# Kernel tuning notes

Hardware: AMD Instinct MI355X
Metric: run time of the kernel (lower is better)

The kernel has to match this reference:

```python
import jax, jax.numpy as jnp
import numpy as np

GRID = 16
N = GRID * GRID          # num_nodes = 256
D = 64                   # embed_dim
SPARSITY = 0.8
BATCH = 2048


def setup_inputs() -> dict:
    key = jax.random.key(0)
    ks = jax.random.split(key, 11)
    s1 = 1.0 / np.sqrt(D)          # fan_in of per-node Linears
    s2 = 1.0 / np.sqrt(N * D)      # fan_in of global_pool first Linear
    x = jax.random.normal(ks[0], (BATCH, N * D), dtype=jnp.float32)
    adj_param = jax.random.normal(ks[1], (N, N), dtype=jnp.float32) * 0.1
    W1 = jax.random.uniform(ks[2], (N, D, D), minval=-s1, maxval=s1, dtype=jnp.float32)
    b1 = jax.random.uniform(ks[3], (N, D), minval=-s1, maxval=s1, dtype=jnp.float32)
    W2 = jax.random.uniform(ks[4], (N, D, D), minval=-s1, maxval=s1, dtype=jnp.float32)
    b2 = jax.random.uniform(ks[5], (N, D), minval=-s1, maxval=s1, dtype=jnp.float32)
    gpW1 = jax.random.uniform(ks[6], (N * D, D), minval=-s2, maxval=s2, dtype=jnp.float32)
    gpb1 = jax.random.uniform(ks[7], (D,), minval=-s2, maxval=s2, dtype=jnp.float32)
    gpW2 = jax.random.uniform(ks[8], (D, D // 2), minval=-s1, maxval=s1, dtype=jnp.float32)
    gpb2 = jax.random.uniform(ks[9], (D // 2,), minval=-s1, maxval=s1, dtype=jnp.float32)
    return {"x": x, "adj_param": adj_param, "W1": W1, "b1": b1, "W2": W2, "b2": b2,
            "gpW1": gpW1, "gpb1": gpb1, "gpW2": gpW2, "gpb2": gpb2}


def _adjacency(adj_param):
    adj = jax.nn.sigmoid(adj_param)
    # threshold = sorted(flat adj)[int(sparsity * N*N)], then hard-threshold, then zero diagonal
    thr = jnp.sort(adj.reshape(-1))[int(SPARSITY * N * N)]
    adj = adj * (adj > thr)
    return adj * (1.0 - jnp.eye(N, dtype=adj.dtype))


def reference(x, adj_param, W1, b1, W2, b2, gpW1, gpb1, gpW2, gpb2):
    B = x.shape[0]
    adj = _adjacency(adj_param)
    xn = x.reshape(B, N, D)                                    # [B, N, D]
    # per-node distinct MLP == grouped GEMM with weights [N, D, D]
    h = jax.nn.relu(jnp.einsum('bnd,nde->bne', xn, W1) + b1)   # [B, N, D]
    node = jnp.einsum('bnd,nde->bne', h, W2) + b2              # [B, N, D]
    # adjacency-weighted neighbor sum: mixed[b,i] = sum_j adj[i,j] * node[b,j]
    mixed = jnp.einsum('ij,bjd->bid', adj, node)               # [B, N, D]
    final = 0.5 * mixed + 0.5 * node                           # residual mix
    g = jax.nn.relu(final.reshape(B, N * D) @ gpW1 + gpb1)     # [B, D]
    out = g @ gpW2 + gpb2                                      # [B, D//2]
    return out, adj
```

## Files before the change

kernel.cpp:

```cpp
#include <hip/hip_runtime.h>
#include <math.h>

typedef unsigned int uint;
typedef unsigned short ushort;
typedef short short8 __attribute__((ext_vector_type(8)));
typedef float f32x4 __attribute__((ext_vector_type(4)));

#define B_ 2048
#define N_ 256
#define D_ 64
#define ND_ 16384
#define NN_ 65536
#define KIDX_ 52428u
#define NGROUPS 16

#define WS_W1T    ((size_t)0)
#define WS_W2T    ((size_t)2*1024*1024)
#define WS_EFF    ((size_t)4*1024*1024)
#define WS_ADJT   ((size_t)6*1024*1024)
#define WS_GPARTS ((size_t)8*1024*1024)
#define WS_SCAL   ((size_t)16*1024*1024)

__device__ __forceinline__ ushort f2bf(float f) {
    uint u = __float_as_uint(f);
    u += 0x7fffu + ((u >> 16) & 1u);
    return (ushort)(u >> 16);
}
__device__ __forceinline__ float bf2f(ushort u) { return __uint_as_float(((uint)u) << 16); }

__device__ __forceinline__ float sigmoid_exact(float a) {
    float t = (float)exp(-(double)a);
    return 1.0f / (1.0f + t);
}

__device__ __forceinline__ int wfrag_off(int e, int k) {
    return ((((e >> 4) * 2 + (k >> 5)) * 4 + ((k >> 3) & 3)) * 16 + (e & 15)) * 8 + (k & 7);
}

__global__ __launch_bounds__(256) void k_convert(const float* __restrict__ W1,
                                                 const float* __restrict__ W2,
                                                 ushort* __restrict__ W1f,
                                                 ushort* __restrict__ W2f) {
    int bid = blockIdx.x, tid = threadIdx.x;
    __shared__ ushort P[4096] __attribute__((aligned(16)));
    const float* src = (bid < 256) ? W1 + (size_t)bid * 4096 : W2 + (size_t)(bid - 256) * 4096;
#pragma unroll
    for (int i = 0; i < 16; i++) {
        int idx = i * 256 + tid;
        int k = idx >> 6, e = idx & 63;
        P[wfrag_off(e, k)] = f2bf(src[idx]);
    }
    __syncthreads();
    ushort* dst = (bid < 256) ? W1f + (size_t)bid * 4096 : W2f + (size_t)(bid - 256) * 4096;
#pragma unroll
    for (int i = 0; i < 2; i++)
        ((uint4*)dst)[i * 256 + tid] = ((const uint4*)P)[i * 256 + tid];
}

__global__ __launch_bounds__(1024, 4) void k_radix_select(const float* __restrict__ adj_param,
                                                          uint* __restrict__ scal) {
    __shared__ uint histL[256 * 64];
    __shared__ uint wsum[4];
    __shared__ uint bc[2];
    int tid = threadIdx.x;
    int lane = tid & 63;
    uint prefix = 0;
    uint rank = KIDX_;
    const uint4* pv = (const uint4*)adj_param;
#pragma unroll 1
    for (int pass = 0; pass < 4; pass++) {
        int shift = 24 - 8 * pass;
        for (int i = tid; i < 256 * 64; i += 1024) histL[i] = 0u;
        __syncthreads();
#pragma unroll 1
        for (int i = 0; i < 16; i++) {
            uint4 b4 = pv[i * 1024 + tid];
#pragma unroll
            for (int c = 0; c < 4; c++) {
                uint bits = (c == 0) ? b4.x : (c == 1) ? b4.y : (c == 2) ? b4.z : b4.w;
                uint key = bits ^ ((bits & 0x80000000u) ? 0xFFFFFFFFu : 0x80000000u);
                bool cand = (pass == 0) || ((key >> (32 - 8 * pass)) == prefix);
                if (cand) atomicAdd(&histL[(((key >> shift) & 0xffu) << 6) + lane], 1u);
            }
        }
        __syncthreads();
        uint s0 = 0, sc = 0;
        if (tid < 256) {
#pragma unroll
            for (int l = 0; l < 64; l++) s0 += histL[(tid << 6) + ((l + tid) & 63)];
            sc = s0;
#pragma unroll
            for (int o = 1; o < 64; o <<= 1) {
                uint t = __shfl_up(sc, o, 64);
                if ((tid & 63) >= o) sc += t;
            }
            if ((tid & 63) == 63) wsum[tid >> 6] = sc;
        }
        __syncthreads();
        if (tid < 256) {
            uint base = 0;
#pragma unroll
            for (int w = 0; w < 4; w++)
                if (w < (tid >> 6)) base += wsum[w];
            uint incl = base + sc;
            uint excl = incl - s0;
            if (excl <= rank && rank < incl) {
                bc[0] = (prefix << 8) | (uint)tid;
                bc[1] = rank - excl;
            }
        }
        __syncthreads();
        prefix = bc[0];
        rank = bc[1];
        __syncthreads();
    }
    if (tid == 0) {
        uint key = prefix;
        uint bits = (key & 0x80000000u) ? (key ^ 0x80000000u) : ~key;
        scal[0] = __float_as_uint(sigmoid_exact(__uint_as_float(bits)));
    }
}

__global__ __launch_bounds__(256) void k_thresh(const float* __restrict__ adj_param,
                                                const uint* __restrict__ scal,
                                                float* __restrict__ adj_out,
                                                ushort* __restrict__ adjTF) {
    int i = blockIdx.x * 256 + threadIdx.x;
    float thr = __uint_as_float(scal[0]);
    float s = sigmoid_exact(adj_param[i]);
    int r = i >> 8, c = i & 255;
    float v = (s > thr && r != c) ? s : 0.0f;
    adj_out[i] = v;
    uint chunk = ((((uint)(c >> 4) * 8u + (uint)(r >> 5)) * 4u + (uint)((r >> 3) & 3)) * 16u + (uint)(c & 15));
    adjTF[chunk * 8u + (uint)(r & 7)] = f2bf(v);
}

__global__ __launch_bounds__(256) void k_eff(const float* __restrict__ gpW1,
                                             const ushort* __restrict__ adjTF,
                                             ushort* __restrict__ effF) {
    __shared__ ushort Bf[16384] __attribute__((aligned(16)));
    int d = blockIdx.x, jt = blockIdx.y, tid = threadIdx.x;
#pragma unroll
    for (int t = 0; t < 16; t++) {
        int idx = t * 256 + tid;
        int i = idx >> 4;
        int f4 = idx & 15;
        float4 v = *(const float4*)(gpW1 + ((size_t)i * 64 + d) * 64 + f4 * 4);
        int slab = i >> 6, il = i & 63, e0 = f4 * 4;
        Bf[slab * 4096 + wfrag_off(e0 + 0, il)] = f2bf(v.x);
        Bf[slab * 4096 + wfrag_off(e0 + 1, il)] = f2bf(v.y);
        Bf[slab * 4096 + wfrag_off(e0 + 2, il)] = f2bf(v.z);
        Bf[slab * 4096 + wfrag_off(e0 + 3, il)] = f2bf(v.w);
    }
    __syncthreads();
    int wid = tid >> 6, lane = tid & 63, quad = lane >> 4, l16 = lane & 15;
    f32x4 acc[4];
#pragma unroll
    for (int nt = 0; nt < 4; nt++) acc[nt] = (f32x4){0.f, 0.f, 0.f, 0.f};
#pragma unroll
    for (int ks8 = 0; ks8 < 8; ks8++) {
        short8 af = *(const short8*)&adjTF[(size_t)(((((jt * 4 + wid) * 8 + ks8) * 4 + quad) * 16 + l16)) * 8];
        int slab = ks8 >> 1, ks = ks8 & 1;
#pragma unroll
        for (int nt = 0; nt < 4; nt++) {
            short8 bf = *(const short8*)&Bf[slab * 4096 + (((nt * 2 + ks) * 4 + quad) * 16 + l16) * 8];
            acc[nt] = __builtin_amdgcn_mfma_f32_16x16x32_bf16(af, bf, acc[nt], 0, 0, 0);
        }
    }
#pragma unroll
    for (int nt = 0; nt < 4; nt++) {
        int e = nt * 16 + l16;
#pragma unroll
        for (int r = 0; r < 4; r++) {
            int j = jt * 64 + wid * 16 + quad * 4 + r;
            float w = gpW1[((size_t)j * 64 + d) * 64 + e];
            float eff = 0.5f * (acc[nt][r] + w);
            effF[(size_t)j * 4096 + wfrag_off(e, d)] = f2bf(eff);
        }
    }
}

__global__ __launch_bounds__(256, 3) void k_fused(const float* __restrict__ x,
                                                  const ushort* __restrict__ W1f,
                                                  const ushort* __restrict__ W2f,
                                                  const ushort* __restrict__ effF,
                                                  const float* __restrict__ b1,
                                                  const float* __restrict__ b2,
                                                  float* __restrict__ gparts) {
    __shared__ ushort Wf1[4096] __attribute__((aligned(16)));
    __shared__ ushort Wf2[4096] __attribute__((aligned(16)));
    __shared__ ushort Ef[4096] __attribute__((aligned(16)));
    __shared__ float Xs[4][16 * 68];
    __shared__ ushort St[4][16 * 72];
    int tid = threadIdx.x;
    int g = blockIdx.x, bt = blockIdx.y;
    int wid = tid >> 6, lane = tid & 63, quad = lane >> 4, l16 = lane & 15;
    int rbase = bt * 64 + wid * 16;
    float* Xw = &Xs[wid][0];
    ushort* Sw = &St[wid][0];

    f32x4 accg[4];
#pragma unroll
    for (int nt = 0; nt < 4; nt++) accg[nt] = (f32x4){0.f, 0.f, 0.f, 0.f};

#pragma unroll 1
    for (int nl = 0; nl < 16; nl++) {
        int n = g * 16 + nl;
        if (nl) __syncthreads();
        {
            const uint4* w1v = (const uint4*)(W1f + (size_t)n * 4096);
            const uint4* w2v = (const uint4*)(W2f + (size_t)n * 4096);
            const uint4* efv = (const uint4*)(effF + (size_t)n * 4096);
            ((uint4*)Wf1)[tid] = w1v[tid];
            ((uint4*)Wf1)[256 + tid] = w1v[256 + tid];
            ((uint4*)Wf2)[tid] = w2v[tid];
            ((uint4*)Wf2)[256 + tid] = w2v[256 + tid];
            ((uint4*)Ef)[tid] = efv[tid];
            ((uint4*)Ef)[256 + tid] = efv[256 + tid];
        }
        float bias1[4], bias2[4];
#pragma unroll
        for (int nt = 0; nt < 4; nt++) {
            bias1[nt] = b1[n * 64 + nt * 16 + l16];
            bias2[nt] = b2[n * 64 + nt * 16 + l16];
        }
        __syncthreads();

#pragma unroll
        for (int i = 0; i < 4; i++) {
            int idx = i * 64 + lane;
            int rl = idx >> 4, seg = idx & 15;
            *(float4*)&Xw[rl * 68 + seg * 4] =
                *(const float4*)(x + (size_t)(rbase + rl) * ND_ + n * 64 + seg * 4);
        }
        short8 fa[2];
        int xr = l16 * 68;
#pragma unroll
        for (int ks = 0; ks < 2; ks++) {
            float4 A = *(const float4*)&Xw[xr + ks * 32 + quad * 8];
            float4 Bq = *(const float4*)&Xw[xr + ks * 32 + quad * 8 + 4];
            short8 a;
            a[0] = (short)f2bf(A.x); a[1] = (short)f2bf(A.y);
            a[2] = (short)f2bf(A.z); a[3] = (short)f2bf(A.w);
            a[4] = (short)f2bf(Bq.x); a[5] = (short)f2bf(Bq.y);
            a[6] = (short)f2bf(Bq.z); a[7] = (short)f2bf(Bq.w);
            fa[ks] = a;
        }
        f32x4 acc[4];
#pragma unroll
        for (int nt = 0; nt < 4; nt++) acc[nt] = (f32x4){0.f, 0.f, 0.f, 0.f};
#pragma unroll
        for (int ks = 0; ks < 2; ks++)
#pragma unroll
            for (int nt = 0; nt < 4; nt++) {
                short8 bf = *(const short8*)&Wf1[(((nt * 2 + ks) * 4 + quad) * 16 + l16) * 8];
                acc[nt] = __builtin_amdgcn_mfma_f32_16x16x32_bf16(fa[ks], bf, acc[nt], 0, 0, 0);
            }
#pragma unroll
        for (int nt = 0; nt < 4; nt++)
#pragma unroll
            for (int r = 0; r < 4; r++) {
                float h = fmaxf(acc[nt][r] + bias1[nt], 0.0f);
                Sw[(quad * 4 + r) * 72 + nt * 16 + l16] = f2bf(h);
            }
        f32x4 acc2[4];
#pragma unroll
        for (int nt = 0; nt < 4; nt++) acc2[nt] = (f32x4){0.f, 0.f, 0.f, 0.f};
#pragma unroll
        for (int ks = 0; ks < 2; ks++) {
            short8 a2 = *(const short8*)&Sw[l16 * 72 + ks * 32 + quad * 8];
#pragma unroll
            for (int nt = 0; nt < 4; nt++) {
                short8 bf = *(const short8*)&Wf2[(((nt * 2 + ks) * 4 + quad) * 16 + l16) * 8];
                acc2[nt] = __builtin_amdgcn_mfma_f32_16x16x32_bf16(a2, bf, acc2[nt], 0, 0, 0);
            }
        }
#pragma unroll
        for (int nt = 0; nt < 4; nt++)
#pragma unroll
            for (int r = 0; r < 4; r++) {
                float v = acc2[nt][r] + bias2[nt];
                Sw[(quad * 4 + r) * 72 + nt * 16 + l16] = f2bf(v);
            }
#pragma unroll
        for (int ks = 0; ks < 2; ks++) {
            short8 a3 = *(const short8*)&Sw[l16 * 72 + ks * 32 + quad * 8];
#pragma unroll
            for (int nt = 0; nt < 4; nt++) {
                short8 bf = *(const short8*)&Ef[(((nt * 2 + ks) * 4 + quad) * 16 + l16) * 8];
                accg[nt] = __builtin_amdgcn_mfma_f32_16x16x32_bf16(a3, bf, accg[nt], 0, 0, 0);
            }
        }
    }
    float* gp = gparts + ((size_t)g * B_ + bt * 64) * 64;
#pragma unroll
    for (int nt = 0; nt < 4; nt++)
#pragma unroll
        for (int r = 0; r < 4; r++) {
            int b_loc = wid * 16 + quad * 4 + r;
            int e = nt * 16 + l16;
            gp[b_loc * 64 + e] = accg[nt][r];
        }
}

__global__ __launch_bounds__(64) void k_gp2(const float* __restrict__ gparts,
                                            const float* __restrict__ gpb1,
                                            const float* __restrict__ gpW2,
                                            const float* __restrict__ gpb2,
                                            float* __restrict__ out) {
    __shared__ float gs[64];
    int b = blockIdx.x, e = threadIdx.x;
    float s = gpb1[e];
#pragma unroll
    for (int p = 0; p < NGROUPS; p++) s += gparts[((size_t)p * B_ + b) * 64 + e];
    gs[e] = fmaxf(s, 0.0f);
    __syncthreads();
    if (e < 32) {
        float a = gpb2[e];
#pragma unroll 8
        for (int k2 = 0; k2 < 64; k2++) a += gs[k2] * gpW2[k2 * 32 + e];
        out[(size_t)b * 32 + e] = a;
    }
}

extern "C" void kernel_launch(void* const* d_in, const int* in_sizes, int n_in,
                              void* d_out, int out_size, void* d_ws, size_t ws_size,
                              hipStream_t stream) {
    const float* x = (const float*)d_in[0];
    const float* adj_param = (const float*)d_in[1];
    const float* W1 = (const float*)d_in[2];
    const float* b1 = (const float*)d_in[3];
    const float* W2 = (const float*)d_in[4];
    const float* b2 = (const float*)d_in[5];
    const float* gpW1 = (const float*)d_in[6];
    const float* gpb1 = (const float*)d_in[7];
    const float* gpW2 = (const float*)d_in[8];
    const float* gpb2 = (const float*)d_in[9];

    float* out = (float*)d_out;
    float* adj_out = (float*)d_out + NN_;

    char* ws = (char*)d_ws;
    ushort* W1f = (ushort*)(ws + WS_W1T);
    ushort* W2f = (ushort*)(ws + WS_W2T);
    ushort* effF = (ushort*)(ws + WS_EFF);
    ushort* adjTF = (ushort*)(ws + WS_ADJT);
    float* gparts = (float*)(ws + WS_GPARTS);
    uint* scal = (uint*)(ws + WS_SCAL);

    k_convert<<<512, 256, 0, stream>>>(W1, W2, W1f, W2f);
    k_radix_select<<<1, 1024, 0, stream>>>(adj_param, scal);
    k_thresh<<<256, 256, 0, stream>>>(adj_param, scal, adj_out, adjTF);
    k_eff<<<dim3(64, 4), 256, 0, stream>>>(gpW1, adjTF, effF);
    k_fused<<<dim3(NGROUPS, 32), 256, 0, stream>>>(x, W1f, W2f, effF, b1, b2, gparts);
    k_gp2<<<2048, 64, 0, stream>>>(gparts, gpb1, gpW2, gpb2, out);
}
```

Baseline: 278.7 us.

## Double-buffer per-node weights via direct global-to-LDS loads and prefetch x

The fused per-node kernel now double-buffers the W1, W2 and effective-pool weight tiles in LDS. The next node's tiles are fetched with global_load_lds while the current node's MFMAs run, and the next x fragments are prefetched into registers, which also removes the LDS staging buffer for x. Biases for all 16 nodes are preloaded into shared memory once. This is meant to hide global load latency and cut one barrier per iteration, at the cost of more LDS and a lower occupancy hint (3 to 2 blocks).

```diff
diff --git a/kernel.cpp b/kernel.cpp
--- a/kernel.cpp
+++ b/kernel.cpp
@@ -35,6 +35,12 @@
 
 __device__ __forceinline__ int wfrag_off(int e, int k) {
     return ((((e >> 4) * 2 + (k >> 5)) * 4 + ((k >> 3) & 3)) * 16 + (e & 15)) * 8 + (k & 7);
+}
+
+__device__ __forceinline__ void glds16(const ushort* g, ushort* l) {
+    __builtin_amdgcn_global_load_lds(
+        (const __attribute__((address_space(1))) ushort*)g,
+        (__attribute__((address_space(3))) ushort*)l, 16, 0, 0);
 }
 
 __global__ __launch_bounds__(256) void k_convert(const float* __restrict__ W1,
@@ -180,82 +186,119 @@
     }
 }
 
-__global__ __launch_bounds__(256, 3) void k_fused(const float* __restrict__ x,
+__global__ __launch_bounds__(256, 2) void k_fused(const float* __restrict__ x,
                                                   const ushort* __restrict__ W1f,
                                                   const ushort* __restrict__ W2f,
                                                   const ushort* __restrict__ effF,
                                                   const float* __restrict__ b1,
                                                   const float* __restrict__ b2,
                                                   float* __restrict__ gparts) {
-    __shared__ ushort Wf1[4096] __attribute__((aligned(16)));
-    __shared__ ushort Wf2[4096] __attribute__((aligned(16)));
-    __shared__ ushort Ef[4096] __attribute__((aligned(16)));
-    __shared__ float Xs[4][16 * 68];
+    __shared__ ushort Wf1[2][4096] __attribute__((aligned(16)));
+    __shared__ ushort Wf2[2][4096] __attribute__((aligned(16)));
+    __shared__ ushort Ef[2][4096] __attribute__((aligned(16)));
     __shared__ ushort St[4][16 * 72];
+    __shared__ float Bs[2][16][64];
     int tid = threadIdx.x;
     int g = blockIdx.x, bt = blockIdx.y;
     int wid = tid >> 6, lane = tid & 63, quad = lane >> 4, l16 = lane & 15;
     int rbase = bt * 64 + wid * 16;
-    float* Xw = &Xs[wid][0];
     ushort* Sw = &St[wid][0];
 
+    {
+        const float* b1g = b1 + (size_t)g * 1024;
+        const float* b2g = b2 + (size_t)g * 1024;
+#pragma unroll
+        for (int i = 0; i < 4; i++) {
+            ((float*)Bs[0])[i * 256 + tid] = b1g[i * 256 + tid];
+            ((float*)Bs[1])[i * 256 + tid] = b2g[i * 256 + tid];
+        }
+    }
+
+    const float* xrow = x + (size_t)(rbase + l16) * ND_ + quad * 8;
+
+    {
+        int n0 = g * 16;
+        int wo = wid * 1024;
+#pragma unroll
+        for (int i = 0; i < 2; i++) {
+            int off = wo + i * 512;
+            glds16(W1f + (size_t)n0 * 4096 + off + lane * 8, &Wf1[0][off]);
+            glds16(W2f + (size_t)n0 * 4096 + off + lane * 8, &Wf2[0][off]);
+            glds16(effF + (size_t)n0 * 4096 + off + lane * 8, &Ef[0][off]);
+        }
+    }
+    float4 xr0, xr1, xr2, xr3;
+    {
+        const float* xp = xrow + (size_t)(g * 16) * 64;
+        xr0 = *(const float4*)(xp);
+        xr1 = *(const float4*)(xp + 4);
+        xr2 = *(const float4*)(xp + 32);
+        xr3 = *(const float4*)(xp + 36);
+    }
+
     f32x4 accg[4];
 #pragma unroll
     for (int nt = 0; nt < 4; nt++) accg[nt] = (f32x4){0.f, 0.f, 0.f, 0.f};
+
+    __syncthreads();
 
 #pragma unroll 1
     for (int nl = 0; nl < 16; nl++) {
-        int n = g * 16 + nl;
-        if (nl) __syncthreads();
+        int cur = nl & 1;
+
+        short8 fa0, fa1;
         {
-            const uint4* w1v = (const uint4*)(W1f + (size_t)n * 4096);
-            const uint4* w2v = (const uint4*)(W2f + (size_t)n * 4096);
-            const uint4* efv = (const uint4*)(effF + (size_t)n * 4096);
-            ((uint4*)Wf1)[tid] = w1v[tid];
-            ((uint4*)Wf1)[256 + tid] = w1v[256 + tid];
-            ((uint4*)Wf2)[tid] = w2v[tid];
-            ((uint4*)Wf2)[256 + tid] = w2v[256 + tid];
-            ((uint4*)Ef)[tid] = efv[tid];
-            ((uint4*)Ef)[256 + tid] = efv[256 + tid];
-        }
+            short8 a;
+            a[0] = (short)f2bf(xr0.x); a[1] = (short)f2bf(xr0.y);
+            a[2] = (short)f2bf(xr0.z); a[3] = (short)f2bf(xr0.w);
+            a[4] = (short)f2bf(xr1.x); a[5] = (short)f2bf(xr1.y);
+            a[6] = (short)f2bf(xr1.z); a[7] = (short)f2bf(xr1.w);
+            fa0 = a;
+            short8 b;
+            b[0] = (short)f2bf(xr2.x); b[1] = (short)f2bf(xr2.y);
+            b[2] = (short)f2bf(xr2.z); b[3] = (short)f2bf(xr2.w);
+            b[4] = (short)f2bf(xr3.x); b[5] = (short)f2bf(xr3.y);
+            b[6] = (short)f2bf(xr3.z); b[7] = (short)f2bf(xr3.w);
+            fa1 = b;
+        }
+
+        if (nl < 15) {
+            int nn = g * 16 + nl + 1;
+            int wo = wid * 1024;
+#pragma unroll
+            for (int i = 0; i < 2; i++) {
+                int off = wo + i * 512;
+                glds16(W1f + (size_t)nn * 4096 + off + lane * 8, &Wf1[cur ^ 1][off]);
+                glds16(W2f + (size_t)nn * 4096 + off + lane * 8, &Wf2[cur ^ 1][off]);
+                glds16(effF + (size_t)nn * 4096 + off + lane * 8, &Ef[cur ^ 1][off]);
+            }
+            const float* xp = xrow + (size_t)nn * 64;
+            xr0 = *(const float4*)(xp);
+            xr1 = *(const float4*)(xp + 4);
+            xr2 = *(const float4*)(xp + 32);
+            xr3 = *(const float4*)(xp + 36);
+        }
+
         float bias1[4], bias2[4];
 #pragma unroll
         for (int nt = 0; nt < 4; nt++) {
-            bias1[nt] = b1[n * 64 + nt * 16 + l16];
-            bias2[nt] = b2[n * 64 + nt * 16 + l16];
-        }
-        __syncthreads();
-
-#pragma unroll
-        for (int i = 0; i < 4; i++) {
-            int idx = i * 64 + lane;
-            int rl = idx >> 4, seg = idx & 15;
-            *(float4*)&Xw[rl * 68 + seg * 4] =
-                *(const float4*)(x + (size_t)(rbase + rl) * ND_ + n * 64 + seg * 4);
-        }
-        short8 fa[2];
-        int xr = l16 * 68;
-#pragma unroll
-        for (int ks = 0; ks < 2; ks++) {
-            float4 A = *(const float4*)&Xw[xr + ks * 32 + quad * 8];
-            float4 Bq = *(const float4*)&Xw[xr + ks * 32 + quad * 8 + 4];
-            short8 a;
-            a[0] = (short)f2bf(A.x); a[1] = (short)f2bf(A.y);
-            a[2] = (short)f2bf(A.z); a[3] = (short)f2bf(A.w);
-            a[4] = (short)f2bf(Bq.x); a[5] = (short)f2bf(Bq.y);
-            a[6] = (short)f2bf(Bq.z); a[7] = (short)f2bf(Bq.w);
-            fa[ks] = a;
-        }
+            bias1[nt] = Bs[0][nl][nt * 16 + l16];
+            bias2[nt] = Bs[1][nl][nt * 16 + l16];
+        }
+
         f32x4 acc[4];
 #pragma unroll
         for (int nt = 0; nt < 4; nt++) acc[nt] = (f32x4){0.f, 0.f, 0.f, 0.f};
 #pragma unroll
-        for (int ks = 0; ks < 2; ks++)
-#pragma unroll
-            for (int nt = 0; nt < 4; nt++) {
-                short8 bf = *(const short8*)&Wf1[(((nt * 2 + ks) * 4 + quad) * 16 + l16) * 8];
-                acc[nt] = __builtin_amdgcn_mfma_f32_16x16x32_bf16(fa[ks], bf, acc[nt], 0, 0, 0);
-            }
+        for (int nt = 0; nt < 4; nt++) {
+            short8 bf = *(const short8*)&Wf1[cur][(((nt * 2 + 0) * 4 + quad) * 16 + l16) * 8];
+            acc[nt] = __builtin_amdgcn_mfma_f32_16x16x32_bf16(fa0, bf, acc[nt], 0, 0, 0);
+        }
+#pragma unroll
+        for (int nt = 0; nt < 4; nt++) {
+            short8 bf = *(const short8*)&Wf1[cur][(((nt * 2 + 1) * 4 + quad) * 16 + l16) * 8];
+            acc[nt] = __builtin_amdgcn_mfma_f32_16x16x32_bf16(fa1, bf, acc[nt], 0, 0, 0);
+        }
 #pragma unroll
         for (int nt = 0; nt < 4; nt++)
 #pragma unroll
@@ -271,7 +314,7 @@
             short8 a2 = *(const short8*)&Sw[l16 * 72 + ks * 32 + quad * 8];
 #pragma unroll
             for (int nt = 0; nt < 4; nt++) {
-                short8 bf = *(const short8*)&Wf2[(((nt * 2 + ks) * 4 + quad) * 16 + l16) * 8];
+                short8 bf = *(const short8*)&Wf2[cur][(((nt * 2 + ks) * 4 + quad) * 16 + l16) * 8];
                 acc2[nt] = __builtin_amdgcn_mfma_f32_16x16x32_bf16(a2, bf, acc2[nt], 0, 0, 0);
             }
         }
@@ -287,11 +330,14 @@
             short8 a3 = *(const short8*)&Sw[l16 * 72 + ks * 32 + quad * 8];
 #pragma unroll
             for (int nt = 0; nt < 4; nt++) {
-                short8 bf = *(const short8*)&Ef[(((nt * 2 + ks) * 4 + quad) * 16 + l16) * 8];
+                short8 bf = *(const short8*)&Ef[cur][(((nt * 2 + ks) * 4 + quad) * 16 + l16) * 8];
                 accg[nt] = __builtin_amdgcn_mfma_f32_16x16x32_bf16(a3, bf, accg[nt], 0, 0, 0);
             }
         }
-    }
+
+        if (nl < 15) __syncthreads();
+    }
+
     float* gp = gparts + ((size_t)g * B_ + bt * 64) * 64;
 #pragma unroll
     for (int nt = 0; nt < 4; nt++)
```

Measured after the change: 278.8 us. No clear change (+0.0%).
